# Optimization experiments

Hardware: AMD Instinct MI355X
Metric: run time of the kernel (lower is better)

Reference implementation:

```python
import jax, jax.numpy as jnp
import numpy as np

B, S, C, H = 2, 2048, 512, 16
D = C // H  # 32
SQRT_DIM = float(np.sqrt(C))  # module scales by sqrt(in_channels), not sqrt(dim)


def setup_inputs() -> dict:
    key = jax.random.key(0)
    ks = jax.random.split(key, 16)
    sc = 1.0 / np.sqrt(C)
    f32 = jnp.float32
    return {
        "q": jax.random.normal(ks[0], (B, S, C), f32),
        "k": jax.random.normal(ks[1], (B, S, C), f32),
        "v": jax.random.normal(ks[2], (B, S, C), f32),
        "pos_embedding": jax.random.normal(ks[3], (B, S, C), f32),
        "Wq": jax.random.normal(ks[4], (C, C), f32) * sc,
        "bq": jnp.zeros((C,), f32),
        "Wk": jax.random.normal(ks[5], (C, C), f32) * sc,
        "bk": jnp.zeros((C,), f32),
        "Wv": jax.random.normal(ks[6], (C, C), f32) * sc,
        "bv": jnp.zeros((C,), f32),
        "Wp": jax.random.normal(ks[7], (C, C), f32) * sc,  # pos_proj has no bias
        "u_bias": jax.random.normal(ks[8], (H, D), f32) * 0.1,
        "v_bias": jax.random.normal(ks[9], (H, D), f32) * 0.1,
        "Wo": jax.random.normal(ks[10], (C, C), f32) * sc,
        "bo": jnp.zeros((C,), f32),
    }


def _skew(pos_score):
    # Transformer-XL pad-shift trick: [B,H,S1,S2] -> relative-shifted scores
    b, h, s1, s2 = pos_score.shape
    zeros = jnp.zeros((b, h, s1, 1), pos_score.dtype)
    padded = jnp.concatenate([zeros, pos_score], axis=-1)  # [b,h,s1,s2+1]
    padded = padded.reshape(b, h, s2 + 1, s1)
    return padded[:, :, 1:].reshape(b, h, s1, s2)


def reference(q, k, v, pos_embedding, Wq, bq, Wk, bk, Wv, bv, Wp, u_bias, v_bias, Wo, bo):
    query = (q @ Wq.T + bq).reshape(B, S, H, D)      # [B,S,H,D]
    key_ = (k @ Wk.T + bk).reshape(B, S, H, D)
    value = (v @ Wv.T + bv).reshape(B, S, H, D)
    pos = (pos_embedding @ Wp.T).reshape(B, S, H, D)
    content = jnp.einsum('bshd,bthd->bhst', query + u_bias, key_)   # [B,H,S,S]
    pos_score = _skew(jnp.einsum('bshd,bthd->bhst', query + v_bias, pos))
    score = (content + pos_score) / SQRT_DIM
    attn = jax.nn.softmax(score, axis=-1)            # dropout_p=0 (eval)
    context = jnp.einsum('bhst,bthd->bshd', attn, value).reshape(B, S, C)
    return context @ Wo.T + bo
```

## Files before the change

### kernel.cpp

```cpp
#include <hip/hip_runtime.h>
#include <math.h>

#define S_ 2048
#define C_ 512
#define H_ 16
#define D_ 32
#define B_ 2
#define M_ (B_ * S_)
#define RSCALE 0.04419417382415922f

typedef __attribute__((ext_vector_type(8))) short bf16x8;
typedef __attribute__((ext_vector_type(4))) float f32x4;

__device__ inline unsigned short f2bf(float f) {
  unsigned u = __builtin_bit_cast(unsigned, f);
  u += 0x7FFFu + ((u >> 16) & 1u);
  return (unsigned short)(u >> 16);
}

__global__ __launch_bounds__(256) void gemm_mfma(
    const float* __restrict__ X, const float* __restrict__ W,
    const float* __restrict__ bias, const float* __restrict__ bias2,
    const float* __restrict__ bias3, float* __restrict__ Of,
    short* __restrict__ Ob, short* __restrict__ Ob2, int mode) {
  __shared__ __align__(16) unsigned short Ah[64][40];
  __shared__ __align__(16) unsigned short Al[64][40];
  __shared__ __align__(16) unsigned short Bh[64][40];
  __shared__ __align__(16) unsigned short Bl[64][40];
  const int tid = threadIdx.x;
  const int w = tid >> 6;
  const int lane = tid & 63;
  const int col = lane & 15;
  const int quad = lane >> 4;
  const int bm = blockIdx.y * 64;
  const int bn = blockIdx.x * 64;
  const int srow = tid >> 2;
  const int skc = (tid & 3) * 8;

  const f32x4 zc = {0.f, 0.f, 0.f, 0.f};
  f32x4 acc[4] = {zc, zc, zc, zc};

  const float* Xp = X + (size_t)(bm + srow) * C_;
  const float* Wp = W + (size_t)(bn + srow) * C_;

  for (int k0 = 0; k0 < C_; k0 += 32) {
    float4 xa = *(const float4*)(Xp + k0 + skc);
    float4 xb = *(const float4*)(Xp + k0 + skc + 4);
    float4 wa = *(const float4*)(Wp + k0 + skc);
    float4 wb = *(const float4*)(Wp + k0 + skc + 4);
    __syncthreads();
    {
      float f[8] = {xa.x, xa.y, xa.z, xa.w, xb.x, xb.y, xb.z, xb.w};
      float g[8] = {wa.x, wa.y, wa.z, wa.w, wb.x, wb.y, wb.z, wb.w};
      unsigned fh[8], fl[8], gh[8], gl[8];
#pragma unroll
      for (int i = 0; i < 8; ++i) {
        unsigned u = __builtin_bit_cast(unsigned, f[i]);
        fh[i] = u & 0xffff0000u;
        fl[i] = __builtin_bit_cast(unsigned, f[i] - __builtin_bit_cast(float, fh[i]));
        unsigned v = __builtin_bit_cast(unsigned, g[i]);
        gh[i] = v & 0xffff0000u;
        gl[i] = __builtin_bit_cast(unsigned, g[i] - __builtin_bit_cast(float, gh[i]));
      }
      uint4 ph, pl, qh, ql;
      ph.x = (fh[0] >> 16) | fh[1];  ph.y = (fh[2] >> 16) | fh[3];
      ph.z = (fh[4] >> 16) | fh[5];  ph.w = (fh[6] >> 16) | fh[7];
      pl.x = (fl[0] >> 16) | (fl[1] & 0xffff0000u);
      pl.y = (fl[2] >> 16) | (fl[3] & 0xffff0000u);
      pl.z = (fl[4] >> 16) | (fl[5] & 0xffff0000u);
      pl.w = (fl[6] >> 16) | (fl[7] & 0xffff0000u);
      qh.x = (gh[0] >> 16) | gh[1];  qh.y = (gh[2] >> 16) | gh[3];
      qh.z = (gh[4] >> 16) | gh[5];  qh.w = (gh[6] >> 16) | gh[7];
      ql.x = (gl[0] >> 16) | (gl[1] & 0xffff0000u);
      ql.y = (gl[2] >> 16) | (gl[3] & 0xffff0000u);
      ql.z = (gl[4] >> 16) | (gl[5] & 0xffff0000u);
      ql.w = (gl[6] >> 16) | (gl[7] & 0xffff0000u);
      *(uint4*)&Ah[srow][skc] = ph;
      *(uint4*)&Al[srow][skc] = pl;
      *(uint4*)&Bh[srow][skc] = qh;
      *(uint4*)&Bl[srow][skc] = ql;
    }
    __syncthreads();
    const bf16x8 ah = *(const bf16x8*)&Ah[16 * w + col][quad * 8];
    const bf16x8 al = *(const bf16x8*)&Al[16 * w + col][quad * 8];
#pragma unroll
    for (int j = 0; j < 4; ++j) {
      const bf16x8 bh = *(const bf16x8*)&Bh[16 * j + col][quad * 8];
      const bf16x8 bl = *(const bf16x8*)&Bl[16 * j + col][quad * 8];
      acc[j] = __builtin_amdgcn_mfma_f32_16x16x32_bf16(ah, bh, acc[j], 0, 0, 0);
      acc[j] = __builtin_amdgcn_mfma_f32_16x16x32_bf16(ah, bl, acc[j], 0, 0, 0);
      acc[j] = __builtin_amdgcn_mfma_f32_16x16x32_bf16(al, bh, acc[j], 0, 0, 0);
    }
  }
#pragma unroll
  for (int j = 0; j < 4; ++j) {
    const int gn = bn + 16 * j + col;
#pragma unroll
    for (int r = 0; r < 4; ++r) {
      const int gm = bm + 16 * w + quad * 4 + r;
      const float a = acc[j][r];
      if (mode == 0) {
        Of[(size_t)gm * C_ + gn] = a + (bias ? bias[gn] : 0.0f);
      } else if (mode == 1) {
        const int h = gn >> 5, d0 = gn & 31;
        const int bb = gm >> 11, s = gm & (S_ - 1);
        const size_t base = ((size_t)(bb * H_ + h) * S_ + s) * D_ + d0;
        const float val = a + bias[gn];
        Ob[base] = (short)f2bf(val + bias2[gn]);
        Ob2[base] = (short)f2bf(val + bias3[gn]);
      } else if (mode == 2) {
        const int h = gn >> 5, d0 = gn & 31;
        const int bb = gm >> 11, s = gm & (S_ - 1);
        Ob[((size_t)(bb * H_ + h) * S_ + s) * D_ + d0] =
            (short)f2bf(a + (bias ? bias[gn] : 0.0f));
      } else {
        const int h = gn >> 5, d0 = gn & 31;
        const int bb = gm >> 11, s = gm & (S_ - 1);
        Ob[((size_t)(bb * H_ + h) * D_ + d0) * S_ + s] =
            (short)f2bf(a + (bias ? bias[gn] : 0.0f));
      }
    }
  }
}

__global__ __launch_bounds__(256, 4) void attn_mfma(
    const short* __restrict__ QU, const short* __restrict__ QV,
    const short* __restrict__ Kb, const short* __restrict__ Vt,
    const short* __restrict__ POSb, float* __restrict__ CTX) {
  __shared__ float PB[64 * 128];
  __shared__ short Pl[64 * 64];
  const int tid = threadIdx.x;
  const int w = tid >> 6;
  const int lane = tid & 63;
  const int col = lane & 15;
  const int quad = lane >> 4;
  const int m0 = blockIdx.x * 64;
  const int bh = blockIdx.y;
  const int b = bh >> 4, h = bh & 15;

  const short* QUh = QU + (size_t)bh * S_ * D_;
  const short* QVh = QV + (size_t)bh * S_ * D_;
  const short* Kh = Kb + (size_t)bh * S_ * D_;
  const short* Vh = Vt + (size_t)bh * D_ * S_;
  const short* Ph = POSb + (size_t)bh * S_ * D_;

  const int arow = m0 + 16 * w + col;
  const bf16x8 aQU = *(const bf16x8*)(QUh + (size_t)arow * D_ + quad * 8);
  const bf16x8 aQVA = *(const bf16x8*)(QVh + (size_t)arow * D_ + quad * 8);
  const bf16x8 aQVB = *(const bf16x8*)(QVh + (size_t)(arow + 1) * D_ + quad * 8);

  const f32x4 zc = {0.f, 0.f, 0.f, 0.f};
  const bf16x8 zb = {0, 0, 0, 0, 0, 0, 0, 0};
  f32x4 ctxa0 = zc, ctxa1 = zc;
  float lpart[4] = {0.f, 0.f, 0.f, 0.f};
  const int mi0 = 16 * w + 4 * quad;

  for (int ch = 0; ch < 32; ++ch) {
    const int n0 = ch * 64;
    const int dnm = n0 - m0;
    f32x4 sc[4];
#pragma unroll
    for (int j = 0; j < 4; ++j) {
      bf16x8 bk = *(const bf16x8*)(Kh + (size_t)(n0 + 16 * j + col) * D_ + quad * 8);
      sc[j] = __builtin_amdgcn_mfma_f32_16x16x32_bf16(aQU, bk, zc, 0, 0, 0);
    }
    if (dnm <= 63) {
      const int tA0 = S_ - 64 + dnm;
#pragma unroll
      for (int j = 0; j < 8; ++j) {
        const int t = tA0 + 16 * j + col;
        bf16x8 bp = *(const bf16x8*)(Ph + (long)t * D_ + quad * 8);
        if (t >= S_) bp = zb;
        f32x4 c = __builtin_amdgcn_mfma_f32_16x16x32_bf16(aQVA, bp, zc, 0, 0, 0);
#pragma unroll
        for (int r = 0; r < 4; ++r) {
          const int mi = mi0 + r;
          const int cc = (16 * j + col) ^ (((mi & 4) << 2) ^ ((mi & 3) << 3));
          PB[mi * 128 + cc] = c[r];
        }
      }
      __syncthreads();
#pragma unroll
      for (int j = 0; j < 4; ++j)
#pragma unroll
        for (int r = 0; r < 4; ++r) {
          const int mi = mi0 + r;
          const int nj = 16 * j + col;
          if (dnm + nj - mi <= 0) {
            const int idx = (nj - mi + 63) ^ (((mi & 4) << 2) ^ ((mi & 3) << 3));
            sc[j][r] += PB[mi * 128 + idx];
          }
        }
    }
    if (dnm >= -61) {
      __syncthreads();
      const int tB0 = dnm - 65;
#pragma unroll
      for (int j = 0; j < 8; ++j) {
        const int t = tB0 + 16 * j + col;
        bf16x8 bp = *(const bf16x8*)(Ph + (long)t * D_ + quad * 8);
        if (t < 0) bp = zb;
        f32x4 c = __builtin_amdgcn_mfma_f32_16x16x32_bf16(aQVB, bp, zc, 0, 0, 0);
#pragma unroll
        for (int r = 0; r < 4; ++r) {
          const int mi = mi0 + r;
          const int cc = (16 * j + col) ^ (((mi & 4) << 2) ^ ((mi & 3) << 3));
          PB[mi * 128 + cc] = c[r];
        }
      }
      __syncthreads();
#pragma unroll
      for (int j = 0; j < 4; ++j)
#pragma unroll
        for (int r = 0; r < 4; ++r) {
          const int mi = mi0 + r;
          const int nj = 16 * j + col;
          if (dnm + nj - mi >= 2) {
            const int idx = (nj - mi + 63) ^ (((mi & 4) << 2) ^ ((mi & 3) << 3));
            sc[j][r] += PB[mi * 128 + idx];
          }
        }
    }
    __syncthreads();
#pragma unroll
    for (int j = 0; j < 4; ++j)
#pragma unroll
      for (int r = 0; r < 4; ++r) {
        const float p = __expf(sc[j][r] * RSCALE);
        lpart[r] += p;
        const int mi = mi0 + r;
        const int cc = (16 * j + col) ^ ((mi & 7) << 3);
        Pl[mi * 64 + cc] = (short)f2bf(p);
      }
    __syncthreads();
    const int prow = 16 * w + col;
    const int psw = (prow & 7) << 3;
#pragma unroll
    for (int k0 = 0; k0 < 2; ++k0) {
      const bf16x8 ap = *(const bf16x8*)(&Pl[prow * 64 + ((k0 * 32 + quad * 8) ^ psw)]);
      bf16x8 bv0 = *(const bf16x8*)(Vh + (size_t)col * S_ + n0 + k0 * 32 + quad * 8);
      ctxa0 = __builtin_amdgcn_mfma_f32_16x16x32_bf16(ap, bv0, ctxa0, 0, 0, 0);
      bf16x8 bv1 = *(const bf16x8*)(Vh + (size_t)(16 + col) * S_ + n0 + k0 * 32 + quad * 8);
      ctxa1 = __builtin_amdgcn_mfma_f32_16x16x32_bf16(ap, bv1, ctxa1, 0, 0, 0);
    }
  }
#pragma unroll
  for (int r = 0; r < 4; ++r) {
    float s = lpart[r];
    s += __shfl_xor(s, 1);
    s += __shfl_xor(s, 2);
    s += __shfl_xor(s, 4);
    s += __shfl_xor(s, 8);
    lpart[r] = 1.0f / s;
  }
  const int mrow = m0 + mi0;
#pragma unroll
  for (int r = 0; r < 4; ++r) {
    const size_t obase = ((size_t)(b * S_ + mrow + r)) * C_ + h * D_;
    CTX[obase + col] = ctxa0[r] * lpart[r];
    CTX[obase + 16 + col] = ctxa1[r] * lpart[r];
  }
}

extern "C" void kernel_launch(void* const* d_in, const int* in_sizes, int n_in,
                              void* d_out, int out_size, void* d_ws, size_t ws_size,
                              hipStream_t stream) {
  (void)in_sizes; (void)n_in; (void)out_size; (void)ws_size;
  const float* q = (const float*)d_in[0];
  const float* k = (const float*)d_in[1];
  const float* v = (const float*)d_in[2];
  const float* pe = (const float*)d_in[3];
  const float* Wq = (const float*)d_in[4];
  const float* bq = (const float*)d_in[5];
  const float* Wk = (const float*)d_in[6];
  const float* bk = (const float*)d_in[7];
  const float* Wv = (const float*)d_in[8];
  const float* bv = (const float*)d_in[9];
  const float* Wp = (const float*)d_in[10];
  const float* ub = (const float*)d_in[11];
  const float* vb = (const float*)d_in[12];
  const float* Wo = (const float*)d_in[13];
  const float* bo = (const float*)d_in[14];
  float* out = (float*)d_out;

  const size_t MC = (size_t)M_ * C_;
  short* QUb = (short*)d_ws;
  short* QVb = QUb + MC;
  short* Kbb = QVb + MC;
  short* Vtb = Kbb + MC;
  short* POSB = Vtb + MC;
  float* CTX = (float*)(POSB + MC);

  dim3 ggrid(C_ / 64, M_ / 64);
  gemm_mfma<<<ggrid, 256, 0, stream>>>(q, Wq, bq, ub, vb, nullptr, QUb, QVb, 1);
  gemm_mfma<<<ggrid, 256, 0, stream>>>(k, Wk, bk, nullptr, nullptr, nullptr, Kbb, nullptr, 2);
  gemm_mfma<<<ggrid, 256, 0, stream>>>(v, Wv, bv, nullptr, nullptr, nullptr, Vtb, nullptr, 3);
  gemm_mfma<<<ggrid, 256, 0, stream>>>(pe, Wp, nullptr, nullptr, nullptr, nullptr, POSB, nullptr, 2);
  attn_mfma<<<dim3(S_ / 64, B_ * H_), 256, 0, stream>>>(QUb, QVb, Kbb, Vtb, POSB, CTX);
  gemm_mfma<<<ggrid, 256, 0, stream>>>(CTX, Wo, bo, nullptr, nullptr, out, nullptr, nullptr, 0);
}
```

Before: 415.0 us.

## Pre-split fp32 inputs to bf16 hi/lo, double-buffer GEMM, batch projections

```diff
diff --git a/kernel.cpp b/kernel.cpp
--- a/kernel.cpp
+++ b/kernel.cpp
@@ -18,80 +18,120 @@
   return (unsigned short)(u >> 16);
 }
 
-__global__ __launch_bounds__(256) void gemm_mfma(
-    const float* __restrict__ X, const float* __restrict__ W,
-    const float* __restrict__ bias, const float* __restrict__ bias2,
-    const float* __restrict__ bias3, float* __restrict__ Of,
-    short* __restrict__ Ob, short* __restrict__ Ob2, int mode) {
-  __shared__ __align__(16) unsigned short Ah[64][40];
-  __shared__ __align__(16) unsigned short Al[64][40];
-  __shared__ __align__(16) unsigned short Bh[64][40];
-  __shared__ __align__(16) unsigned short Bl[64][40];
+__global__ __launch_bounds__(256) void split_x(
+    const float* __restrict__ q, const float* __restrict__ k,
+    const float* __restrict__ v, const float* __restrict__ pe,
+    short* __restrict__ xh, short* __restrict__ xl) {
+  const int z = blockIdx.y;
+  const float* src = z == 0 ? q : z == 1 ? k : z == 2 ? v : pe;
+  const size_t off = (size_t)z * M_ * C_;
+  const size_t i = ((size_t)blockIdx.x * 256 + threadIdx.x) * 4;
+  float4 f = *(const float4*)(src + i);
+  float ff[4] = {f.x, f.y, f.z, f.w};
+  ushort4 hv, lv;
+  unsigned short* ph = (unsigned short*)&hv;
+  unsigned short* pl = (unsigned short*)&lv;
+#pragma unroll
+  for (int e = 0; e < 4; ++e) {
+    unsigned u = __builtin_bit_cast(unsigned, ff[e]);
+    unsigned hi = u & 0xffff0000u;
+    ph[e] = (unsigned short)(hi >> 16);
+    pl[e] = f2bf(ff[e] - __builtin_bit_cast(float, hi));
+  }
+  *(ushort4*)(xh + off + i) = hv;
+  *(ushort4*)(xl + off + i) = lv;
+}
+
+__global__ __launch_bounds__(256) void split_w(
+    const float* __restrict__ w0, const float* __restrict__ w1,
+    const float* __restrict__ w2, const float* __restrict__ w3,
+    const float* __restrict__ w4, short* __restrict__ wh,
+    short* __restrict__ wl) {
+  const int z = blockIdx.y;
+  const float* src = z == 0 ? w0 : z == 1 ? w1 : z == 2 ? w2 : z == 3 ? w3 : w4;
+  const size_t off = (size_t)z * C_ * C_;
+  const size_t i = ((size_t)blockIdx.x * 256 + threadIdx.x) * 4;
+  float4 f = *(const float4*)(src + i);
+  float ff[4] = {f.x, f.y, f.z, f.w};
+  ushort4 hv, lv;
+  unsigned short* ph = (unsigned short*)&hv;
+  unsigned short* pl = (unsigned short*)&lv;
+#pragma unroll
+  for (int e = 0; e < 4; ++e) {
+    unsigned u = __builtin_bit_cast(unsigned, ff[e]);
+    unsigned hi = u & 0xffff0000u;
+    ph[e] = (unsigned short)(hi >> 16);
+    pl[e] = f2bf(ff[e] - __builtin_bit_cast(float, hi));
+  }
+  *(ushort4*)(wh + off + i) = hv;
+  *(ushort4*)(wl + off + i) = lv;
+}
+
+__device__ __forceinline__ void gemm_core(
+    const short* __restrict__ Xh, const short* __restrict__ Xl,
+    const short* __restrict__ Wh, const short* __restrict__ Wl,
+    const float* bias, const float* bias2, const float* bias3,
+    float* __restrict__ Of, short* __restrict__ Ob, short* __restrict__ Ob2,
+    int mode) {
+  __shared__ __align__(16) short LAh[2][64 * 72];
+  __shared__ __align__(16) short LAl[2][64 * 72];
+  __shared__ __align__(16) short LBh[2][64 * 72];
+  __shared__ __align__(16) short LBl[2][64 * 72];
   const int tid = threadIdx.x;
-  const int w = tid >> 6;
-  const int lane = tid & 63;
-  const int col = lane & 15;
-  const int quad = lane >> 4;
-  const int bm = blockIdx.y * 64;
-  const int bn = blockIdx.x * 64;
-  const int srow = tid >> 2;
-  const int skc = (tid & 3) * 8;
-
+  const int w = tid >> 6, lane = tid & 63, col = lane & 15, quad = lane >> 4;
+  const int bm = blockIdx.y * 64, bn = blockIdx.x * 64;
   const f32x4 zc = {0.f, 0.f, 0.f, 0.f};
   f32x4 acc[4] = {zc, zc, zc, zc};
 
-  const float* Xp = X + (size_t)(bm + srow) * C_;
-  const float* Wp = W + (size_t)(bn + srow) * C_;
-
-  for (int k0 = 0; k0 < C_; k0 += 32) {
-    float4 xa = *(const float4*)(Xp + k0 + skc);
-    float4 xb = *(const float4*)(Xp + k0 + skc + 4);
-    float4 wa = *(const float4*)(Wp + k0 + skc);
-    float4 wb = *(const float4*)(Wp + k0 + skc + 4);
+  uint4 rah[2], ral[2], rbh[2], rbl[2];
+  const int r0 = tid >> 3, c0 = (tid & 7) * 8;
+  const int r1 = (tid + 256) >> 3, c1 = c0;
+#define LOAD_REGS(k0)                                                     \
+  {                                                                       \
+    rah[0] = *(const uint4*)(Xh + (size_t)(bm + r0) * C_ + (k0) + c0);    \
+    ral[0] = *(const uint4*)(Xl + (size_t)(bm + r0) * C_ + (k0) + c0);    \
+    rbh[0] = *(const uint4*)(Wh + (size_t)(bn + r0) * C_ + (k0) + c0);    \
+    rbl[0] = *(const uint4*)(Wl + (size_t)(bn + r0) * C_ + (k0) + c0);    \
+    rah[1] = *(const uint4*)(Xh + (size_t)(bm + r1) * C_ + (k0) + c1);    \
+    ral[1] = *(const uint4*)(Xl + (size_t)(bm + r1) * C_ + (k0) + c1);    \
+    rbh[1] = *(const uint4*)(Wh + (size_t)(bn + r1) * C_ + (k0) + c1);    \
+    rbl[1] = *(const uint4*)(Wl + (size_t)(bn + r1) * C_ + (k0) + c1);    \
+  }
+#define STORE_LDS(buf)                                                    \
+  {                                                                       \
+    *(uint4*)&LAh[buf][r0 * 72 + c0] = rah[0];                            \
+    *(uint4*)&LAl[buf][r0 * 72 + c0] = ral[0];                            \
+    *(uint4*)&LBh[buf][r0 * 72 + c0] = rbh[0];                            \
+    *(uint4*)&LBl[buf][r0 * 72 + c0] = rbl[0];                            \
+    *(uint4*)&LAh[buf][r1 * 72 + c1] = rah[1];                            \
+    *(uint4*)&LAl[buf][r1 * 72 + c1] = ral[1];                            \
+    *(uint4*)&LBh[buf][r1 * 72 + c1] = rbh[1];                            \
+    *(uint4*)&LBl[buf][r1 * 72 + c1] = rbl[1];                            \
+  }
+  LOAD_REGS(0)
+  STORE_LDS(0)
+  for (int it = 0; it < 8; ++it) {
     __syncthreads();
-    {
-      float f[8] = {xa.x, xa.y, xa.z, xa.w, xb.x, xb.y, xb.z, xb.w};
-      float g[8] = {wa.x, wa.y, wa.z, wa.w, wb.x, wb.y, wb.z, wb.w};
-      unsigned fh[8], fl[8], gh[8], gl[8];
-#pragma unroll
-      for (int i = 0; i < 8; ++i) {
-        unsigned u = __builtin_bit_cast(unsigned, f[i]);
-        fh[i] = u & 0xffff0000u;
-        fl[i] = __builtin_bit_cast(unsigned, f[i] - __builtin_bit_cast(float, fh[i]));
-        unsigned v = __builtin_bit_cast(unsigned, g[i]);
-        gh[i] = v & 0xffff0000u;
-        gl[i] = __builtin_bit_cast(unsigned, g[i] - __builtin_bit_cast(float, gh[i]));
-      }
-      uint4 ph, pl, qh, ql;
-      ph.x = (fh[0] >> 16) | fh[1];  ph.y = (fh[2] >> 16) | fh[3];
-      ph.z = (fh[4] >> 16) | fh[5];  ph.w = (fh[6] >> 16) | fh[7];
-      pl.x = (fl[0] >> 16) | (fl[1] & 0xffff0000u);
-      pl.y = (fl[2] >> 16) | (fl[3] & 0xffff0000u);
-      pl.z = (fl[4] >> 16) | (fl[5] & 0xffff0000u);
-      pl.w = (fl[6] >> 16) | (fl[7] & 0xffff0000u);
-      qh.x = (gh[0] >> 16) | gh[1];  qh.y = (gh[2] >> 16) | gh[3];
-      qh.z = (gh[4] >> 16) | gh[5];  qh.w = (gh[6] >> 16) | gh[7];
-      ql.x = (gl[0] >> 16) | (gl[1] & 0xffff0000u);
-      ql.y = (gl[2] >> 16) | (gl[3] & 0xffff0000u);
-      ql.z = (gl[4] >> 16) | (gl[5] & 0xffff0000u);
-      ql.w = (gl[6] >> 16) | (gl[7] & 0xffff0000u);
-      *(uint4*)&Ah[srow][skc] = ph;
-      *(uint4*)&Al[srow][skc] = pl;
-      *(uint4*)&Bh[srow][skc] = qh;
-      *(uint4*)&Bl[srow][skc] = ql;
-    }
-    __syncthreads();
-    const bf16x8 ah = *(const bf16x8*)&Ah[16 * w + col][quad * 8];
-    const bf16x8 al = *(const bf16x8*)&Al[16 * w + col][quad * 8];
-#pragma unroll
-    for (int j = 0; j < 4; ++j) {
-      const bf16x8 bh = *(const bf16x8*)&Bh[16 * j + col][quad * 8];
-      const bf16x8 bl = *(const bf16x8*)&Bl[16 * j + col][quad * 8];
-      acc[j] = __builtin_amdgcn_mfma_f32_16x16x32_bf16(ah, bh, acc[j], 0, 0, 0);
-      acc[j] = __builtin_amdgcn_mfma_f32_16x16x32_bf16(ah, bl, acc[j], 0, 0, 0);
-      acc[j] = __builtin_amdgcn_mfma_f32_16x16x32_bf16(al, bh, acc[j], 0, 0, 0);
-    }
-  }
+    if (it < 7) LOAD_REGS((it + 1) * 64)
+    const int buf = it & 1;
+#pragma unroll
+    for (int ks = 0; ks < 2; ++ks) {
+      const int ko = ks * 32 + quad * 8;
+      const bf16x8 ah = *(const bf16x8*)&LAh[buf][(16 * w + col) * 72 + ko];
+      const bf16x8 al = *(const bf16x8*)&LAl[buf][(16 * w + col) * 72 + ko];
+#pragma unroll
+      for (int j = 0; j < 4; ++j) {
+        const bf16x8 bh = *(const bf16x8*)&LBh[buf][(16 * j + col) * 72 + ko];
+        const bf16x8 bl = *(const bf16x8*)&LBl[buf][(16 * j + col) * 72 + ko];
+        acc[j] = __builtin_amdgcn_mfma_f32_16x16x32_bf16(ah, bh, acc[j], 0, 0, 0);
+        acc[j] = __builtin_amdgcn_mfma_f32_16x16x32_bf16(ah, bl, acc[j], 0, 0, 0);
+        acc[j] = __builtin_amdgcn_mfma_f32_16x16x32_bf16(al, bh, acc[j], 0, 0, 0);
+      }
+    }
+    if (it < 7) STORE_LDS(1 - buf)
+  }
+#undef LOAD_REGS
+#undef STORE_LDS
 #pragma unroll
   for (int j = 0; j < 4; ++j) {
     const int gn = bn + 16 * j + col;
@@ -123,10 +163,40 @@
   }
 }
 
+__global__ __launch_bounds__(256, 2) void proj4(
+    const short* __restrict__ XH, const short* __restrict__ XL,
+    const short* __restrict__ WH, const short* __restrict__ WL,
+    const float* bq, const float* bkk, const float* bvv,
+    const float* ub, const float* vb,
+    short* QU, short* QV, short* Kb, short* Vt, short* POS) {
+  const int z = blockIdx.z;
+  const size_t MC = (size_t)M_ * C_, WC = (size_t)C_ * C_;
+  const short* xh = XH + z * MC;
+  const short* xl = XL + z * MC;
+  const short* wh = WH + z * WC;
+  const short* wl = WL + z * WC;
+  const float* b1 = z == 0 ? bq : z == 1 ? bkk : z == 2 ? bvv : nullptr;
+  const int mode = z == 0 ? 1 : z == 2 ? 3 : 2;
+  short* ob = z == 0 ? QU : z == 1 ? Kb : z == 2 ? Vt : POS;
+  short* ob2 = z == 0 ? QV : nullptr;
+  gemm_core(xh, xl, wh, wl, b1, z == 0 ? ub : nullptr, z == 0 ? vb : nullptr,
+            nullptr, ob, ob2, mode);
+}
+
+__global__ __launch_bounds__(256, 2) void gemm_out(
+    const short* __restrict__ CTXh, const short* __restrict__ CTXl,
+    const short* __restrict__ WH, const short* __restrict__ WL,
+    const float* bo, float* __restrict__ out) {
+  const size_t WC = (size_t)C_ * C_;
+  gemm_core(CTXh, CTXl, WH + 4 * WC, WL + 4 * WC, bo, nullptr, nullptr,
+            out, nullptr, nullptr, 0);
+}
+
 __global__ __launch_bounds__(256, 4) void attn_mfma(
     const short* __restrict__ QU, const short* __restrict__ QV,
     const short* __restrict__ Kb, const short* __restrict__ Vt,
-    const short* __restrict__ POSb, float* __restrict__ CTX) {
+    const short* __restrict__ POSb, short* __restrict__ CTXh,
+    short* __restrict__ CTXl) {
   __shared__ float PB[64 * 128];
   __shared__ short Pl[64 * 64];
   const int tid = threadIdx.x;
@@ -257,8 +327,14 @@
 #pragma unroll
   for (int r = 0; r < 4; ++r) {
     const size_t obase = ((size_t)(b * S_ + mrow + r)) * C_ + h * D_;
-    CTX[obase + col] = ctxa0[r] * lpart[r];
-    CTX[obase + 16 + col] = ctxa1[r] * lpart[r];
+    const float v0 = ctxa0[r] * lpart[r];
+    const float v1 = ctxa1[r] * lpart[r];
+    const unsigned u0 = __builtin_bit_cast(unsigned, v0) & 0xffff0000u;
+    const unsigned u1 = __builtin_bit_cast(unsigned, v1) & 0xffff0000u;
+    CTXh[obase + col] = (short)(u0 >> 16);
+    CTXl[obase + col] = (short)f2bf(v0 - __builtin_bit_cast(float, u0));
+    CTXh[obase + 16 + col] = (short)(u1 >> 16);
+    CTXl[obase + 16 + col] = (short)f2bf(v1 - __builtin_bit_cast(float, u1));
   }
 }
 
@@ -284,18 +360,24 @@
   float* out = (float*)d_out;
 
   const size_t MC = (size_t)M_ * C_;
-  short* QUb = (short*)d_ws;
+  const size_t WC = (size_t)C_ * C_;
+  short* XH = (short*)d_ws;
+  short* XL = XH + 4 * MC;
+  short* WH = XL + 4 * MC;
+  short* WL = WH + 5 * WC;
+  short* QUb = WL + 5 * WC;
   short* QVb = QUb + MC;
   short* Kbb = QVb + MC;
   short* Vtb = Kbb + MC;
   short* POSB = Vtb + MC;
-  float* CTX = (float*)(POSB + MC);
-
-  dim3 ggrid(C_ / 64, M_ / 64);
-  gemm_mfma<<<ggrid, 256, 0, stream>>>(q, Wq, bq, ub, vb, nullptr, QUb, QVb, 1);
-  gemm_mfma<<<ggrid, 256, 0, stream>>>(k, Wk, bk, nullptr, nullptr, nullptr, Kbb, nullptr, 2);
-  gemm_mfma<<<ggrid, 256, 0, stream>>>(v, Wv, bv, nullptr, nullptr, nullptr, Vtb, nullptr, 3);
-  gemm_mfma<<<ggrid, 256, 0, stream>>>(pe, Wp, nullptr, nullptr, nullptr, nullptr, POSB, nullptr, 2);
-  attn_mfma<<<dim3(S_ / 64, B_ * H_), 256, 0, stream>>>(QUb, QVb, Kbb, Vtb, POSB, CTX);
-  gemm_mfma<<<ggrid, 256, 0, stream>>>(CTX, Wo, bo, nullptr, nullptr, out, nullptr, nullptr, 0);
-}
+  short* CTXh = POSB + MC;
+  short* CTXl = CTXh + MC;
+
+  split_x<<<dim3(2048, 4), 256, 0, stream>>>(q, k, v, pe, XH, XL);
+  split_w<<<dim3(256, 5), 256, 0, stream>>>(Wq, Wk, Wv, Wp, Wo, WH, WL);
+  proj4<<<dim3(8, 64, 4), 256, 0, stream>>>(XH, XL, WH, WL, bq, bk, bv, ub, vb,
+                                            QUb, QVb, Kbb, Vtb, POSB);
+  attn_mfma<<<dim3(S_ / 64, B_ * H_), 256, 0, stream>>>(QUb, QVb, Kbb, Vtb, POSB,
+                                                        CTXh, CTXl);
+  gemm_out<<<dim3(8, 64), 256, 0, stream>>>(CTXh, CTXl, WH, WL, bo, out);
+}
```

Measured after the change: 371.1 us. -10.6%, faster.
